# Kernel optimization log

Hardware: AMD Instinct MI355X
Metric: run time of the kernel (lower is better)

The kernel has to match this reference:

```python
import jax, jax.numpy as jnp
import numpy as np

B, N, D = 16, 8192, 384   # examples, sentences per example, embedding dim
KN = 16                   # neighbors per node (kNN degree)
K, H, STEPS = 8, 128, 3   # coin dim, hidden dim, walk steps


def setup_inputs() -> dict:
    key = jax.random.key(0)
    ks = jax.random.split(key, 12)
    s = 0.02
    return {
        "sent_embs": jax.random.normal(ks[0], (B, N, D), dtype=jnp.float32),
        "q_embs": jax.random.normal(ks[1], (B, D), dtype=jnp.float32),
        "neighbors": jax.random.randint(ks[2], (B, N, KN), 0, N, dtype=jnp.int32),
        # coin_net: Linear(2D->H), ReLU, Linear(H->K)
        "coin_w1": jax.random.normal(ks[3], (2 * D, H), dtype=jnp.float32) * s,
        "coin_b1": jnp.zeros((H,), dtype=jnp.float32),
        "coin_w2": jax.random.normal(ks[4], (H, K), dtype=jnp.float32) * s,
        "coin_b2": jnp.zeros((K,), dtype=jnp.float32),
        # path_net: Linear(D+K+D->H), ReLU, Linear(H->1)
        "path_w1": jax.random.normal(ks[5], (D + K + D, H), dtype=jnp.float32) * s,
        "path_b1": jnp.zeros((H,), dtype=jnp.float32),
        "path_w2": jax.random.normal(ks[6], (H, 1), dtype=jnp.float32) * s,
        "path_b2": jnp.zeros((1,), dtype=jnp.float32),
    }


def _mlp(x, w1, b1, w2, b2):
    return jax.nn.relu(x @ w1 + b1) @ w2 + b2


def _forward(sent_embs, q_embs, neighbors,
             coin_w1, coin_b1, coin_w2, coin_b2,
             path_w1, path_b1, path_w2, path_b2):
    b, n, d = sent_embs.shape
    k = coin_w2.shape[1]
    q_bcast = jnp.broadcast_to(q_embs[:, None, :], (b, n, d))

    # coin amplitudes per node: [B, N, K]
    amps = _mlp(jnp.concatenate([sent_embs, q_bcast], axis=-1),
                coin_w1, coin_b1, coin_w2, coin_b2)

    # initial uniform walk state: 1/sqrt(N*K)
    state = jnp.full((b, n, k), 1.0 / np.sqrt(n * k), dtype=sent_embs.dtype)

    # adjacency = self-loop + edges row -> neighbors[row]; A @ X == X + masked neighbor gather-sum
    valid = (neighbors >= 0) & (neighbors < n)           # [B, N, KN]
    safe_nbrs = jnp.where(valid, neighbors, 0)
    batch_idx = jnp.arange(b)[:, None, None]

    for _ in range(STEPS):
        ns = state * amps                                # coin step
        gathered = ns[batch_idx, safe_nbrs]              # [B, N, KN, K]
        gathered = jnp.where(valid[..., None], gathered, 0.0)
        ns = ns + gathered.sum(axis=2)                   # sparse.mm(A, ns)
        norm = jnp.linalg.norm(ns.reshape(b, -1), axis=1)[:, None, None]
        state = ns / jnp.where(norm > 0, norm, 1.0)      # renormalize (guard norm==0)

    path_in = jnp.concatenate([sent_embs, state, q_bcast], axis=-1)  # [B, N, D+K+D]
    logits = _mlp(path_in, path_w1, path_b1, path_w2, path_b2)[..., 0]  # [B, N]
    return logits


def reference(sent_embs, q_embs, neighbors,
              coin_w1, coin_b1, coin_w2, coin_b2,
              path_w1, path_b1, path_w2, path_b2):
    return _forward(sent_embs, q_embs, neighbors,
                    coin_w1, coin_b1, coin_w2, coin_b2,
                    path_w1, path_b1, path_w2, path_b2)
```

## Files before the change

### kernel.cpp

```cpp
#include <hip/hip_runtime.h>

#define B_SZ 16
#define N_SZ 8192
#define D_SZ 384
#define KN_SZ 16
#define K_SZ 8
#define H_SZ 128
#define M_TOTAL (B_SZ * N_SZ)
#define KSTEPS 12
#define TROWS 32
#define NT (M_TOTAL / TROWS)
#define LDSA_STRIDE 400
#define HTS 132
#define GEMM_GRID 512

typedef short short8 __attribute__((ext_vector_type(8)));
typedef short short4v __attribute__((ext_vector_type(4)));
typedef float floatx4 __attribute__((ext_vector_type(4)));

__device__ __forceinline__ unsigned short f2bf(float f) {
    unsigned u = __builtin_bit_cast(unsigned, f);
    u += 0x7FFFu + ((u >> 16) & 1u);
    return (unsigned short)(u >> 16);
}
__device__ __forceinline__ float bf2f(unsigned short b) {
    unsigned u = ((unsigned)b) << 16;
    return __builtin_bit_cast(float, u);
}

__global__ void prep_kernel(const float* __restrict__ q_embs,
                            const float* __restrict__ coin_w1,
                            const float* __restrict__ coin_b1,
                            const float* __restrict__ path_w1,
                            const float* __restrict__ path_b1,
                            unsigned short* __restrict__ wswz,
                            float* __restrict__ qcoin, float* __restrict__ qpath,
                            float* __restrict__ norms) {
    int blk = blockIdx.x;
    int t = threadIdx.x;
    if (blk < 384) {
        int f = blk * 256 + t;
        int j  = f & 7;
        int l  = (f >> 3) & 63;
        int ss = (f >> 9) % KSTEPS;
        int ct = f / (KSTEPS * 512);
        int k = ss * 32 + ((l >> 4) << 3) + j;
        int n = ct * 16 + (l & 15);
        float v = (n < H_SZ) ? coin_w1[k * H_SZ + n]
                             : path_w1[k * H_SZ + (n - H_SZ)];
        wswz[f] = f2bf(v);
    } else if (blk == 384) {
        if (t < B_SZ) norms[t] = 0.f;
    } else {
        int b = blk - 385;
        const float* q = q_embs + b * D_SZ;
        if (t < H_SZ) {
            float acc = coin_b1[t];
            for (int d = 0; d < D_SZ; d++)
                acc += q[d] * coin_w1[(D_SZ + d) * H_SZ + t];
            qcoin[b * H_SZ + t] = acc;
        } else if (t < 2 * H_SZ) {
            int h = t - H_SZ;
            float acc = path_b1[h];
            for (int d = 0; d < D_SZ; d++)
                acc += q[d] * path_w1[(D_SZ + K_SZ + d) * H_SZ + h];
            qpath[b * H_SZ + h] = acc;
        }
    }
}

__global__ __launch_bounds__(256, 2)
void gemm_fused(const float* __restrict__ sent,
                const unsigned short* __restrict__ wswz,
                const float* __restrict__ qcoin,
                const float* __restrict__ coin_w2,
                const float* __restrict__ coin_b2,
                unsigned short* __restrict__ hpathB,
                float* __restrict__ amps,
                float* __restrict__ z0) {
    __shared__ short als[TROWS * LDSA_STRIDE];
    __shared__ float htile[TROWS * HTS];
    __shared__ float w2s[H_SZ * K_SZ];
    __shared__ float qcs[H_SZ];
    __shared__ float b2s[K_SZ];
    const int tid = threadIdx.x;
    const int wave = tid >> 6, lane = tid & 63;
    const int m_lane = lane & 15, quad = lane >> 4;

    for (int i = tid; i < H_SZ * K_SZ; i += 256) w2s[i] = coin_w2[i];
    if (tid < K_SZ) b2s[tid] = coin_b2[tid];

    short8 bfrag[4][KSTEPS];
#pragma unroll
    for (int c = 0; c < 4; c++) {
        int ct = wave * 4 + c;
#pragma unroll
        for (int s = 0; s < KSTEPS; s++)
            bfrag[c][s] = *(const short8*)(wswz + ((((ct * KSTEPS + s) * 64) + lane) << 3));
    }

    const int colw = (wave & 1) * 64;
    const int is_path = (wave >= 2);

    for (int mt = blockIdx.x; mt < NT; mt += GEMM_GRID) {
        const int b = mt >> 8;
        const float* abase = sent + (size_t)mt * TROWS * D_SZ;
#pragma unroll
        for (int cc = 0; cc < 3; cc++) {
            float4 v[4];
#pragma unroll
            for (int u = 0; u < 4; u++)
                v[u] = *(const float4*)(abase + (size_t)((cc * 4 + u) * 256 + tid) * 4);
#pragma unroll
            for (int u = 0; u < 4; u++) {
                int e4 = (cc * 4 + u) * 256 + tid;
                int row = e4 / 96;
                int c4  = e4 - row * 96;
                short4v sv;
                sv.x = (short)f2bf(v[u].x); sv.y = (short)f2bf(v[u].y);
                sv.z = (short)f2bf(v[u].z); sv.w = (short)f2bf(v[u].w);
                *(short4v*)&als[row * LDSA_STRIDE + c4 * 4] = sv;
            }
        }
        if (tid < H_SZ) qcs[tid] = qcoin[b * H_SZ + tid];
        __syncthreads();

#pragma unroll
        for (int rt = 0; rt < 2; rt++) {
            floatx4 acc[4];
#pragma unroll
            for (int c = 0; c < 4; c++) acc[c] = (floatx4){0.f, 0.f, 0.f, 0.f};
#pragma unroll
            for (int s = 0; s < KSTEPS; s++) {
                short8 afrag = *(const short8*)&als[(rt * 16 + m_lane) * LDSA_STRIDE + s * 32 + quad * 8];
#pragma unroll
                for (int c = 0; c < 4; c++)
                    acc[c] = __builtin_amdgcn_mfma_f32_16x16x32_bf16(afrag, bfrag[c][s], acc[c], 0, 0, 0);
            }
            if (!is_path) {
#pragma unroll
                for (int c = 0; c < 4; c++) {
                    int col = colw + c * 16 + m_lane;
#pragma unroll
                    for (int r = 0; r < 4; r++)
                        htile[(rt * 16 + quad * 4 + r) * HTS + col] = acc[c][r];
                }
            } else {
                int mt16 = mt * 2 + rt;
#pragma unroll
                for (int c = 0; c < 4; c++) {
                    int col = colw + c * 16 + m_lane;
                    short4v sv;
                    sv.x = (short)f2bf(acc[c][0]); sv.y = (short)f2bf(acc[c][1]);
                    sv.z = (short)f2bf(acc[c][2]); sv.w = (short)f2bf(acc[c][3]);
                    *(short4v*)(hpathB + (size_t)mt16 * 2048 + col * 16 + quad * 4) = sv;
                }
            }
        }
        __syncthreads();

        {
            const int row = tid >> 3, hg = tid & 7;
            float pa[K_SZ];
#pragma unroll
            for (int j = 0; j < K_SZ; j++) pa[j] = 0.f;
#pragma unroll
            for (int k = 0; k < 16; k++) {
                int h = hg + 8 * k;
                float hv = htile[row * HTS + h] + qcs[h];
                hv = hv > 0.f ? hv : 0.f;
                float4 wa = *(const float4*)&w2s[h * 8];
                float4 wb = *(const float4*)&w2s[h * 8 + 4];
                pa[0] += hv * wa.x; pa[1] += hv * wa.y; pa[2] += hv * wa.z; pa[3] += hv * wa.w;
                pa[4] += hv * wb.x; pa[5] += hv * wb.y; pa[6] += hv * wb.z; pa[7] += hv * wb.w;
            }
#pragma unroll
            for (int o = 1; o < 8; o <<= 1) {
#pragma unroll
                for (int j = 0; j < K_SZ; j++) pa[j] += __shfl_xor(pa[j], o);
            }
            if ((tid & 7) == 0) {
                const float c0 = 1.0f / 256.0f;
                int m = mt * TROWS + row;
#pragma unroll
                for (int j = 0; j < K_SZ; j++) pa[j] += b2s[j];
                float4 o0 = {pa[0], pa[1], pa[2], pa[3]};
                float4 o1 = {pa[4], pa[5], pa[6], pa[7]};
                *(float4*)(amps + (size_t)m * 8)     = o0;
                *(float4*)(amps + (size_t)m * 8 + 4) = o1;
                float4 s0 = {pa[0]*c0, pa[1]*c0, pa[2]*c0, pa[3]*c0};
                float4 s1 = {pa[4]*c0, pa[5]*c0, pa[6]*c0, pa[7]*c0};
                *(float4*)(z0 + (size_t)m * 8)     = s0;
                *(float4*)(z0 + (size_t)m * 8 + 4) = s1;
            }
        }
        __syncthreads();
    }
}

__global__ __launch_bounds__(256)
void walk_step(const float* __restrict__ z,
               const int* __restrict__ neighbors,
               const float* __restrict__ amps,
               float* __restrict__ outz,
               float* __restrict__ norms, int last) {
    const int g = blockIdx.x * 256 + threadIdx.x;
    const int m = g >> 1, half = g & 1;
    const int b = m >> 13;
    const size_t nbase = (size_t)b << 13;
    const int off = half * 4;

    float4 v = *(const float4*)(z + (size_t)m * 8 + off);
    int nbr[KN_SZ];
    const int4* nb4 = (const int4*)(neighbors + (size_t)m * KN_SZ);
#pragma unroll
    for (int i = 0; i < 4; i++) *(int4*)&nbr[i * 4] = nb4[i];
#pragma unroll
    for (int i = 0; i < KN_SZ; i++) {
        int nn = nbr[i];
        if (nn >= 0 && nn < N_SZ) {
            float4 gv = *(const float4*)(z + (nbase + nn) * 8 + off);
            v.x += gv.x; v.y += gv.y; v.z += gv.z; v.w += gv.w;
        }
    }
    if (!last) {
        float4 a = *(const float4*)(amps + (size_t)m * 8 + off);
        v.x *= a.x; v.y *= a.y; v.z *= a.z; v.w *= a.w;
        *(float4*)(outz + (size_t)m * 8 + off) = v;
    } else {
        *(float4*)(outz + (size_t)m * 8 + off) = v;
        float ss = v.x * v.x + v.y * v.y + v.z * v.z + v.w * v.w;
#pragma unroll
        for (int o = 32; o > 0; o >>= 1) ss += __shfl_down(ss, o);
        __shared__ float blocksum;
        if (threadIdx.x == 0) blocksum = 0.f;
        __syncthreads();
        if ((threadIdx.x & 63) == 0) atomicAdd(&blocksum, ss);
        __syncthreads();
        if (threadIdx.x == 0) atomicAdd(&norms[b], blocksum);
    }
}

__global__ __launch_bounds__(256)
void logits_kernel(const unsigned short* __restrict__ hpathB,
                   const float* __restrict__ qpath,
                   const float* __restrict__ u2,
                   const float* __restrict__ norms,
                   const float* __restrict__ path_w1,
                   const float* __restrict__ path_w2,
                   const float* __restrict__ path_b2,
                   float* __restrict__ out) {
    __shared__ float w1t[H_SZ * K_SZ];
    __shared__ float w2s[H_SZ];
    __shared__ float qps[H_SZ];
    const int tid = threadIdx.x;
    const int m = blockIdx.x * 256 + tid;
    const int b = (blockIdx.x * 256) >> 13;
    for (int i = tid; i < K_SZ * H_SZ; i += 256) {
        int h = i >> 3, j = i & 7;
        w1t[i] = path_w1[(D_SZ + j) * H_SZ + h];
    }
    if (tid < H_SZ) { w2s[tid] = path_w2[tid]; qps[tid] = qpath[b * H_SZ + tid]; }
    __syncthreads();

    float ssq = norms[b];
    float inv = ssq > 0.f ? rsqrtf(ssq) : 1.0f;
    float st[K_SZ];
    {
        float4 s0 = *(const float4*)(u2 + (size_t)m * 8);
        float4 s1 = *(const float4*)(u2 + (size_t)m * 8 + 4);
        st[0] = s0.x * inv; st[1] = s0.y * inv; st[2] = s0.z * inv; st[3] = s0.w * inv;
        st[4] = s1.x * inv; st[5] = s1.y * inv; st[6] = s1.z * inv; st[7] = s1.w * inv;
    }

    const unsigned short* hb = hpathB + (size_t)(m >> 4) * 2048 + (m & 15);
    float acc = path_b2[0];
    for (int h = 0; h < H_SZ; h++) {
        float hv = bf2f(hb[h * 16]) + qps[h];
        float4 wa = *(const float4*)&w1t[h * 8];
        float4 wb = *(const float4*)&w1t[h * 8 + 4];
        hv += st[0]*wa.x + st[1]*wa.y + st[2]*wa.z + st[3]*wa.w
            + st[4]*wb.x + st[5]*wb.y + st[6]*wb.z + st[7]*wb.w;
        hv = hv > 0.f ? hv : 0.f;
        acc += hv * w2s[h];
    }
    out[m] = acc;
}

extern "C" void kernel_launch(void* const* d_in, const int* in_sizes, int n_in,
                              void* d_out, int out_size, void* d_ws, size_t ws_size,
                              hipStream_t stream) {
    const float* sent      = (const float*)d_in[0];
    const float* q_embs    = (const float*)d_in[1];
    const int*   neighbors = (const int*)d_in[2];
    const float* coin_w1   = (const float*)d_in[3];
    const float* coin_b1   = (const float*)d_in[4];
    const float* coin_w2   = (const float*)d_in[5];
    const float* coin_b2   = (const float*)d_in[6];
    const float* path_w1   = (const float*)d_in[7];
    const float* path_b1   = (const float*)d_in[8];
    const float* path_w2   = (const float*)d_in[9];
    const float* path_b2   = (const float*)d_in[10];
    float* out = (float*)d_out;

    char* ws = (char*)d_ws;
    unsigned short* wswz = (unsigned short*)ws;
    float* qcoin = (float*)(ws + 196608);
    float* qpath = (float*)(ws + 196608 + 8192);
    float* norms = (float*)(ws + 196608 + 16384);
    unsigned short* hpathB = (unsigned short*)(ws + 213248);
    float* amps = (float*)(ws + 213248 + 33554432ull);
    float* zA   = amps + (size_t)M_TOTAL * K_SZ;
    float* zB   = zA   + (size_t)M_TOTAL * K_SZ;

    prep_kernel<<<401, 256, 0, stream>>>(q_embs, coin_w1, coin_b1, path_w1, path_b1,
                                         wswz, qcoin, qpath, norms);
    gemm_fused<<<GEMM_GRID, 256, 0, stream>>>(sent, wswz, qcoin, coin_w2, coin_b2,
                                              hpathB, amps, zA);
    walk_step<<<2 * M_TOTAL / 256, 256, 0, stream>>>(zA, neighbors, amps, zB, norms, 0);
    walk_step<<<2 * M_TOTAL / 256, 256, 0, stream>>>(zB, neighbors, amps, zA, norms, 0);
    walk_step<<<2 * M_TOTAL / 256, 256, 0, stream>>>(zA, neighbors, amps, zB, norms, 1);
    logits_kernel<<<M_TOTAL / 256, 256, 0, stream>>>(hpathB, qpath, zB, norms,
                                                     path_w1, path_w2, path_b2, out);
}
```

Baseline: 482.7 us.

## Use 64-row GEMM tiles with register prefetch of next tile

The fused GEMM now processes 64-row tiles instead of 32. The next tile's activations are prefetched into registers while the current tile runs its MFMAs. B fragments are no longer held in registers for the whole kernel; they are reloaded from global/L2 at each k-step. The coin hidden tile is stored transposed in LDS as bf16, and the reduction uses 4 threads per row. This aims to overlap global loads with compute and raise MFMA reuse of each A/B fragment. The costs are high register pressure (24 float4 prefetch registers plus 16 accumulators), lost occupancy from removing the launch-bounds minimum, and one barrier removed per loop iteration.

```diff
diff --git a/kernel.cpp b/kernel.cpp
--- a/kernel.cpp
+++ b/kernel.cpp
@@ -8,11 +8,11 @@
 #define H_SZ 128
 #define M_TOTAL (B_SZ * N_SZ)
 #define KSTEPS 12
-#define TROWS 32
-#define NT (M_TOTAL / TROWS)
+#define MT64 (M_TOTAL / 64)
+#define GEMM_GRID 512
+#define TILES_PB (MT64 / GEMM_GRID)
 #define LDSA_STRIDE 400
-#define HTS 132
-#define GEMM_GRID 512
+#define HT_STRIDE 66
 
 typedef short short8 __attribute__((ext_vector_type(8)));
 typedef short short4v __attribute__((ext_vector_type(4)));
@@ -69,7 +69,7 @@
     }
 }
 
-__global__ __launch_bounds__(256, 2)
+__global__ __launch_bounds__(256)
 void gemm_fused(const float* __restrict__ sent,
                 const unsigned short* __restrict__ wswz,
                 const float* __restrict__ qcoin,
@@ -78,96 +78,115 @@
                 unsigned short* __restrict__ hpathB,
                 float* __restrict__ amps,
                 float* __restrict__ z0) {
-    __shared__ short als[TROWS * LDSA_STRIDE];
-    __shared__ float htile[TROWS * HTS];
+    __shared__ short als[64 * LDSA_STRIDE];
+    __shared__ unsigned short htile[H_SZ * HT_STRIDE];
     __shared__ float w2s[H_SZ * K_SZ];
     __shared__ float qcs[H_SZ];
     __shared__ float b2s[K_SZ];
     const int tid = threadIdx.x;
     const int wave = tid >> 6, lane = tid & 63;
     const int m_lane = lane & 15, quad = lane >> 4;
+    const int blk = blockIdx.x;
 
     for (int i = tid; i < H_SZ * K_SZ; i += 256) w2s[i] = coin_w2[i];
     if (tid < K_SZ) b2s[tid] = coin_b2[tid];
 
-    short8 bfrag[4][KSTEPS];
-#pragma unroll
-    for (int c = 0; c < 4; c++) {
-        int ct = wave * 4 + c;
-#pragma unroll
-        for (int s = 0; s < KSTEPS; s++)
-            bfrag[c][s] = *(const short8*)(wswz + ((((ct * KSTEPS + s) * 64) + lane) << 3));
-    }
-
+    const unsigned short* wbase = wswz + (size_t)wave * 4 * KSTEPS * 512 + lane * 8;
     const int colw = (wave & 1) * 64;
-    const int is_path = (wave >= 2);
-
-    for (int mt = blockIdx.x; mt < NT; mt += GEMM_GRID) {
-        const int b = mt >> 8;
-        const float* abase = sent + (size_t)mt * TROWS * D_SZ;
-#pragma unroll
-        for (int cc = 0; cc < 3; cc++) {
-            float4 v[4];
-#pragma unroll
-            for (int u = 0; u < 4; u++)
-                v[u] = *(const float4*)(abase + (size_t)((cc * 4 + u) * 256 + tid) * 4);
-#pragma unroll
-            for (int u = 0; u < 4; u++) {
-                int e4 = (cc * 4 + u) * 256 + tid;
-                int row = e4 / 96;
-                int c4  = e4 - row * 96;
-                short4v sv;
-                sv.x = (short)f2bf(v[u].x); sv.y = (short)f2bf(v[u].y);
-                sv.z = (short)f2bf(v[u].z); sv.w = (short)f2bf(v[u].w);
-                *(short4v*)&als[row * LDSA_STRIDE + c4 * 4] = sv;
-            }
-        }
-        if (tid < H_SZ) qcs[tid] = qcoin[b * H_SZ + tid];
+
+    float4 v[24];
+    {
+        const float* ab = sent + (size_t)blk * 64 * D_SZ;
+#pragma unroll
+        for (int u = 0; u < 24; u++)
+            v[u] = *(const float4*)(ab + (size_t)(u * 256 + tid) * 4);
+    }
+
+    for (int t = 0; t < TILES_PB; t++) {
+        const int mt = blk + t * GEMM_GRID;
+        const int b = mt >> 7;
+
+#pragma unroll
+        for (int u = 0; u < 24; u++) {
+            int e4 = u * 256 + tid;
+            int row = e4 / 96;
+            int c4  = e4 - row * 96;
+            short4v sv;
+            sv.x = (short)f2bf(v[u].x); sv.y = (short)f2bf(v[u].y);
+            sv.z = (short)f2bf(v[u].z); sv.w = (short)f2bf(v[u].w);
+            *(short4v*)&als[row * LDSA_STRIDE + c4 * 4] = sv;
+        }
         __syncthreads();
 
-#pragma unroll
-        for (int rt = 0; rt < 2; rt++) {
-            floatx4 acc[4];
-#pragma unroll
-            for (int c = 0; c < 4; c++) acc[c] = (floatx4){0.f, 0.f, 0.f, 0.f};
-#pragma unroll
-            for (int s = 0; s < KSTEPS; s++) {
-                short8 afrag = *(const short8*)&als[(rt * 16 + m_lane) * LDSA_STRIDE + s * 32 + quad * 8];
+        if (t + 1 < TILES_PB) {
+            const float* ab = sent + (size_t)(blk + (t + 1) * GEMM_GRID) * 64 * D_SZ;
+#pragma unroll
+            for (int u = 0; u < 24; u++)
+                v[u] = *(const float4*)(ab + (size_t)(u * 256 + tid) * 4);
+        }
+
+        floatx4 acc[4][4];
+#pragma unroll
+        for (int rt = 0; rt < 4; rt++)
+#pragma unroll
+            for (int c = 0; c < 4; c++) acc[rt][c] = (floatx4){0.f, 0.f, 0.f, 0.f};
+
+#pragma unroll
+        for (int s = 0; s < KSTEPS; s++) {
+            short8 bf[4];
+#pragma unroll
+            for (int c = 0; c < 4; c++)
+                bf[c] = *(const short8*)(wbase + (size_t)(c * KSTEPS + s) * 512);
+            short8 af[4];
+#pragma unroll
+            for (int rt = 0; rt < 4; rt++)
+                af[rt] = *(const short8*)&als[(rt * 16 + m_lane) * LDSA_STRIDE + s * 32 + quad * 8];
+#pragma unroll
+            for (int rt = 0; rt < 4; rt++)
 #pragma unroll
                 for (int c = 0; c < 4; c++)
-                    acc[c] = __builtin_amdgcn_mfma_f32_16x16x32_bf16(afrag, bfrag[c][s], acc[c], 0, 0, 0);
-            }
-            if (!is_path) {
+                    acc[rt][c] = __builtin_amdgcn_mfma_f32_16x16x32_bf16(af[rt], bf[c], acc[rt][c], 0, 0, 0);
+        }
+
+        if (wave < 2) {
+#pragma unroll
+            for (int rt = 0; rt < 4; rt++) {
 #pragma unroll
                 for (int c = 0; c < 4; c++) {
                     int col = colw + c * 16 + m_lane;
-#pragma unroll
-                    for (int r = 0; r < 4; r++)
-                        htile[(rt * 16 + quad * 4 + r) * HTS + col] = acc[c][r];
+                    int row0 = rt * 16 + quad * 4;
+                    short4v sv;
+                    sv.x = (short)f2bf(acc[rt][c][0]); sv.y = (short)f2bf(acc[rt][c][1]);
+                    sv.z = (short)f2bf(acc[rt][c][2]); sv.w = (short)f2bf(acc[rt][c][3]);
+                    *(short4v*)&htile[col * HT_STRIDE + row0] = sv;
                 }
-            } else {
-                int mt16 = mt * 2 + rt;
+            }
+        } else {
+#pragma unroll
+            for (int rt = 0; rt < 4; rt++) {
+                int mt16 = mt * 4 + rt;
 #pragma unroll
                 for (int c = 0; c < 4; c++) {
                     int col = colw + c * 16 + m_lane;
                     short4v sv;
-                    sv.x = (short)f2bf(acc[c][0]); sv.y = (short)f2bf(acc[c][1]);
-                    sv.z = (short)f2bf(acc[c][2]); sv.w = (short)f2bf(acc[c][3]);
+                    sv.x = (short)f2bf(acc[rt][c][0]); sv.y = (short)f2bf(acc[rt][c][1]);
+                    sv.z = (short)f2bf(acc[rt][c][2]); sv.w = (short)f2bf(acc[rt][c][3]);
                     *(short4v*)(hpathB + (size_t)mt16 * 2048 + col * 16 + quad * 4) = sv;
                 }
             }
         }
+        if (tid < H_SZ) qcs[tid] = qcoin[b * H_SZ + tid];
         __syncthreads();
 
         {
-            const int row = tid >> 3, hg = tid & 7;
+            const int row = tid >> 2, hp = tid & 3;
             float pa[K_SZ];
 #pragma unroll
             for (int j = 0; j < K_SZ; j++) pa[j] = 0.f;
-#pragma unroll
-            for (int k = 0; k < 16; k++) {
-                int h = hg + 8 * k;
-                float hv = htile[row * HTS + h] + qcs[h];
+#pragma unroll 4
+            for (int k = 0; k < 32; k++) {
+                int h = hp * 32 + k;
+                float hv = bf2f(htile[h * HT_STRIDE + row]) + qcs[h];
                 hv = hv > 0.f ? hv : 0.f;
                 float4 wa = *(const float4*)&w2s[h * 8];
                 float4 wb = *(const float4*)&w2s[h * 8 + 4];
@@ -175,13 +194,13 @@
                 pa[4] += hv * wb.x; pa[5] += hv * wb.y; pa[6] += hv * wb.z; pa[7] += hv * wb.w;
             }
 #pragma unroll
-            for (int o = 1; o < 8; o <<= 1) {
-#pragma unroll
-                for (int j = 0; j < K_SZ; j++) pa[j] += __shfl_xor(pa[j], o);
-            }
-            if ((tid & 7) == 0) {
+            for (int j = 0; j < K_SZ; j++) {
+                pa[j] += __shfl_xor(pa[j], 1);
+                pa[j] += __shfl_xor(pa[j], 2);
+            }
+            if (hp == 0) {
                 const float c0 = 1.0f / 256.0f;
-                int m = mt * TROWS + row;
+                int m = mt * 64 + row;
 #pragma unroll
                 for (int j = 0; j < K_SZ; j++) pa[j] += b2s[j];
                 float4 o0 = {pa[0], pa[1], pa[2], pa[3]};
@@ -194,7 +213,6 @@
                 *(float4*)(z0 + (size_t)m * 8 + 4) = s1;
             }
         }
-        __syncthreads();
     }
 }
 
```

New measurement: 429.9 us. 1.12x faster.
